# Optimization experiments

Measured on AMD Instinct MI355X. Metric: run time of the kernel, lower is better.

The kernel has to match this reference:

```python
import jax, jax.numpy as jnp
import numpy as np
from jax import lax

N = 5000
C = 81  # num_classes including background at index 0
BG_OFFSET = 1


def _iou_matrix(b):
    # b: [N,4] as x1,y1,x2,y2 -> pairwise IoU [N,N]
    x1, y1, x2, y2 = b[:, 0], b[:, 1], b[:, 2], b[:, 3]
    area = (x2 - x1) * (y2 - y1)  # [N]
    ix1 = jnp.maximum(x1[:, None], x1[None, :])
    iy1 = jnp.maximum(y1[:, None], y1[None, :])
    ix2 = jnp.minimum(x2[:, None], x2[None, :])
    iy2 = jnp.minimum(y2[:, None], y2[None, :])
    iw = jnp.maximum(ix2 - ix1, 0.0)
    ih = jnp.maximum(iy2 - iy1, 0.0)
    inter = iw * ih
    return inter / (area[:, None] + area[None, :] - inter)


def setup_inputs() -> dict:
    key = jax.random.key(0)
    k1, k2, k3 = jax.random.split(key, 3)
    # valid boxes: x1<x2, y1<y2 on a ~1024px canvas, size ~up to 256px
    xy1 = jax.random.uniform(k1, (N, 2), dtype=jnp.float32) * 1024.0
    wh = jax.random.uniform(k2, (N, 2), dtype=jnp.float32) * 256.0 + 1.0
    bboxes = jnp.concatenate([xy1, xy1 + wh], axis=1)  # [N,4]
    scores = jax.random.uniform(k3, (N, C), dtype=jnp.float32)  # [N,C]
    return {
        "bboxes": bboxes,
        "scores": scores,
        "conf_thresh": 0.6,
        "nms_thresh": 0.5,
        "max_instances": 300,
    }


def _multiclass_nms(bboxes, scores, conf_thresh, nms_thresh, max_instances):
    n = bboxes.shape[0]
    neg_inf = jnp.finfo(scores.dtype).min
    iou = _iou_matrix(bboxes)  # [N,N]

    def nms_one_class(score_c):  # score_c: [N]
        valid = score_c > conf_thresh
        masked = jnp.where(valid, score_c, neg_inf)
        order = jnp.argsort(masked)[::-1]  # descending score

        def step(suppressed, idx):
            keep = valid[idx] & ~suppressed[idx]
            new_sup = jnp.where(keep, suppressed | (iou[idx] > nms_thresh), suppressed)
            return new_sup, keep

        _, keeps = lax.scan(step, jnp.zeros((n,), bool), order)
        # scatter keep flags back to original box order
        return jnp.zeros((n,), bool).at[order].set(keeps)

    fg_scores = scores[:, BG_OFFSET:].T  # [C-1, N]
    keep = jax.vmap(nms_one_class)(fg_scores)  # [C-1, N]

    # global top-k over all (class, box) kept detections, sorted by score desc
    flat = jnp.where(keep, fg_scores, neg_inf).reshape(-1)  # [(C-1)*N]
    top_scores, top_idx = lax.top_k(flat, max_instances)
    cls = top_idx // n + BG_OFFSET  # [K]
    box = top_idx % n  # [K]
    valid_out = top_scores > neg_inf / 2

    sel_score = scores[box, cls]  # differentiable gather
    preds = jnp.concatenate([bboxes[box], sel_score[:, None]], axis=1)  # [K,5]
    preds = jnp.where(valid_out[:, None], preds, 0.0)
    labels = jnp.where(valid_out, cls, -1)
    return preds, labels


def reference(bboxes, scores, conf_thresh, nms_thresh, max_instances):
    return _multiclass_nms(bboxes, scores, conf_thresh, nms_thresh, max_instances)
```

## Files before the change

### kernel.cpp

```cpp
#include <hip/hip_runtime.h>

typedef unsigned long long u64;
typedef unsigned int u32;
typedef unsigned short u16;

#define MSORT 4096
#define TPB1  1024
#define TPBF  1024
#define BOXCAP 3648
#define KCAP  3072
#define RSLOT_W 10
#define KPC   300
#define SELCAP 1024
#define PREFR 64
#define TBOX  128

#define WG_SCOPE  __HIP_MEMORY_SCOPE_WORKGROUP
#define DEV_SCOPE __HIP_MEMORY_SCOPE_AGENT

__device__ __forceinline__ float boxArea(float4 b) {
    return __fmul_rn(__fsub_rn(b.z, b.x), __fsub_rn(b.w, b.y));
}

template<bool GE>
__device__ __forceinline__ bool iou_gt(float4 a, float area_a, float4 b, float area_b, double B) {
    float ix1 = fmaxf(a.x, b.x), iy1 = fmaxf(a.y, b.y);
    float ix2 = fminf(a.z, b.z), iy2 = fminf(a.w, b.w);
    float iw  = fmaxf(__fsub_rn(ix2, ix1), 0.0f);
    float ih  = fmaxf(__fsub_rn(iy2, iy1), 0.0f);
    float inter = __fmul_rn(iw, ih);
    float uni   = __fsub_rn(__fadd_rn(area_a, area_b), inter);
    return GE ? ((double)inter >= B * (double)uni) : ((double)inter > B * (double)uni);
}

__device__ __forceinline__ int scoreBin(u32 bits) {
    int b = (int)(bits >> 12) - 0x3F000;
    return b < 0 ? 0 : (b > 2047 ? 2047 : b);
}

__device__ __forceinline__ void bstar_wave0(
    const u32* __restrict__ hist, int target, int tid,
    int* __restrict__ outBs, int* __restrict__ outTot)
{
    if (tid < 64) {
        int s = 0;
        #pragma unroll
        for (int b = 0; b < 32; b++)
            s += (int)hist[(tid << 5) + ((b + tid) & 31)];
        #pragma unroll
        for (int d = 1; d < 64; d <<= 1) {
            int v = __shfl_down(s, d, 64);
            if (tid + d < 64) s += v;
        }
        u64 bal = __ballot(s >= target);
        int ch  = bal ? (63 - __builtin_clzll(bal)) : -1;
        int tot = __shfl(s, 0, 64);
        int bs  = 0;
        if (ch >= 0) {
            int accAbove = (ch < 63) ? __shfl(s, ch + 1, 64) : 0;
            int h = (tid < 32) ? (int)hist[(ch << 5) + tid] : 0;
            #pragma unroll
            for (int d = 1; d < 32; d <<= 1) {
                int v = __shfl_down(h, d, 64);
                if (tid + d < 32) h += v;
            }
            u64 bal2 = __ballot((tid < 32) && (accAbove + h >= target));
            bs = (ch << 5) + (63 - __builtin_clzll(bal2));
        }
        if (tid == 0) { *outBs = bs; if (outTot) *outTot = tot; }
    }
}

__global__ __launch_bounds__(1024) void transpose_kernel(
    const float* __restrict__ scores, int N, int C,
    float* __restrict__ scoresT, u32* __restrict__ gHist)
{
    __shared__ float tile[TBOX * 81];
    const int tid = threadIdx.x;
    const int b0  = blockIdx.x * TBOX;
    const int nb  = (N - b0 < TBOX) ? (N - b0) : TBOX;
    const int tot = nb * C;
    for (int e = tid; e < tot; e += 1024)
        tile[e] = scores[(size_t)b0 * C + e];
    __syncthreads();
    if (nb == TBOX) {
        const int wtot = C << 7;
        for (int o = tid; o < wtot; o += 1024) {
            int cls = o >> 7, j = o & (TBOX - 1);
            scoresT[(size_t)cls * N + b0 + j] = tile[j * C + cls];
        }
    } else {
        const int wtot = C * nb;
        for (int o = tid; o < wtot; o += 1024) {
            int cls = o / nb, j = o - cls * nb;
            scoresT[(size_t)cls * N + b0 + j] = tile[j * C + cls];
        }
    }
    if (blockIdx.x == 0)
        for (int h = tid; h < 2052; h += 1024) gHist[h] = 0;
}

template<bool GE>
__device__ __forceinline__ int prefix_nms_w0(
    const float* __restrict__ bboxes, const u64* __restrict__ sorted,
    int R, double B, int tid, int c, int N, u64* __restrict__ gkept_c,
    u32* __restrict__ gHist)
{
    u64 key = (tid < R) ? sorted[tid] : 0;
    float4 bx = make_float4(0.f, 0.f, 0.f, 0.f);
    if (tid < R) bx = ((const float4*)bboxes)[(u32)key];
    float ar = boxArea(bx);
    u64 supB = (R >= 64) ? 0ull : (~0ull << R);
    int nk = 0;
    int i = -1;
    for (;;) {
        u64 mask = (i >= 63) ? 0ull : (~0ull << (i + 1));
        u64 alive = ~supB & mask;
        if (!alive) break;
        i = (int)__builtin_ctzll(alive);
        float4 bi;
        bi.x = __shfl(bx.x, i, 64); bi.y = __shfl(bx.y, i, 64);
        bi.z = __shfl(bx.z, i, 64); bi.w = __shfl(bx.w, i, 64);
        float ai = boxArea(bi);
        if (tid == 0) {
            u64 ki = sorted[i];
            u32 flat = (u32)c * (u32)N + (u32)ki;
            gkept_c[nk] = (ki & 0xFFFFFFFF00000000ull) | (u32)(~flat);
        }
        nk++;
        bool sup = (tid > i) && iou_gt<GE>(bi, ai, bx, ar, B);
        supB |= __ballot(sup);
    }
    if (tid < R && !((supB >> tid) & 1ull))
        atomicAdd(&gHist[scoreBin((u32)(key >> 32))], 1u);
    return nk;
}

__global__ __launch_bounds__(TPB1, 1) void nms_select_kernel(
    const float* __restrict__ bboxes, const float* __restrict__ scoresT,
    const float* __restrict__ conf_ptr, const float* __restrict__ nms_ptr,
    int N, u64* __restrict__ gkept,
    u32* __restrict__ gK, u32* __restrict__ g65, u32* __restrict__ gPre,
    u32* __restrict__ gHist, u32* __restrict__ gNk)
{
    __shared__ u64 keys[KCAP];
    __shared__ u32 hist[2048];
    __shared__ u64 keybuf[256];
    __shared__ u64 sorted[66];
    __shared__ int cntS, ncollS, bstarS, nkS;

    const int tid  = threadIdx.x;
    const int lane = tid & 63;
    const int c    = blockIdx.x;
    const int cls  = c + 1;
    const float conf = *conf_ptr;
    const float nmsT = *nms_ptr;

    for (int b = tid; b < 2048; b += TPB1) hist[b] = 0;
    if (tid < 66) sorted[tid] = 0;
    if (tid == 0) { cntS = 0; ncollS = 0; nkS = 0; }
    __syncthreads();

    const float* rowT = scoresT + (size_t)cls * N;
    const float4* rowT4 = (const float4*)rowT;
    const int N4 = N >> 2;
    for (int i4 = tid; i4 < N4; i4 += TPB1) {
        float4 s4 = rowT4[i4];
        #pragma unroll
        for (int j = 0; j < 4; j++) {
            float s = (j == 0) ? s4.x : (j == 1) ? s4.y : (j == 2) ? s4.z : s4.w;
            bool pass = (s > conf);
            u64 m = __ballot(pass);
            if (m) {
                int leader = (int)__builtin_ctzll(m);
                int base = 0;
                if (lane == leader) base = atomicAdd(&cntS, __popcll(m));
                base = __shfl(base, leader, 64);
                if (pass) {
                    int p = base + (int)__popcll(m & ((1ull << lane) - 1ull));
                    if (p < KCAP)
                        keys[p] = ((u64)__float_as_uint(s) << 32) | (u32)((i4 << 2) + j);
                    atomicAdd(&hist[scoreBin(__float_as_uint(s))], 1u);
                }
            }
        }
    }
    for (int i = (N4 << 2) + tid; i < N; i += TPB1) {
        float s = rowT[i];
        if (s > conf) {
            int p = atomicAdd(&cntS, 1);
            if (p < KCAP) keys[p] = ((u64)__float_as_uint(s) << 32) | (u32)i;
            atomicAdd(&hist[scoreBin(__float_as_uint(s))], 1u);
        }
    }
    __syncthreads();
    const int K = cntS;
    const bool preOv = (K > KCAP);
    const int target = K < (PREFR + 1) ? K : (PREFR + 1);

    bstar_wave0(hist, target, tid, &bstarS, nullptr);
    __syncthreads();
    const u32 tbits = (bstarS == 0) ? 0u : (((u32)bstarS + 0x3F000u) << 12);

    const int KL = K < KCAP ? K : KCAP;
    for (int p = tid; p < KL; p += TPB1) {
        u64 k = keys[p];
        bool pass = ((u32)(k >> 32) >= tbits);
        u64 m = __ballot(pass);
        if (m) {
            int leader = (int)__builtin_ctzll(m);
            int base = 0;
            if (lane == leader) base = atomicAdd(&ncollS, (int)__popcll(m));
            base = __shfl(base, leader, 64);
            if (pass) {
                int pos = base + (int)__popcll(m & ((1ull << lane) - 1ull));
                if (pos < 256) keybuf[pos] = k;
            }
        }
    }
    __syncthreads();
    const int ncoll = ncollS;
    const bool pre = preOv || (ncoll > 256);
    for (int p = ncoll + tid; p < 256; p += TPB1) keybuf[p] = 0;
    __syncthreads();

    u64* gkept_c = gkept + (size_t)c * KPC;
    if (!pre) {
        if (tid < 256) {
            u64 my = keybuf[tid];
            int rank = 0;
            for (int j = 0; j < 256; j++) rank += (keybuf[j] > my);
            if (my && rank < PREFR + 1) sorted[rank] = my;
        }
        __syncthreads();
        const u32 tb = __float_as_uint(nmsT);
        const float Tn = __uint_as_float(tb + 1u);
        const double B = ((double)nmsT + (double)Tn) * 0.5;
        const bool geCmp = (((tb + 1u) & 1u) == 0u);
        if (tid < 64) {
            int R = ncoll < PREFR ? ncoll : PREFR;
            int nk = geCmp ? prefix_nms_w0<true >(bboxes, sorted, R, B, tid, c, N, gkept_c, gHist)
                           : prefix_nms_w0<false>(bboxes, sorted, R, B, tid, c, N, gkept_c, gHist);
            if (tid == 0) nkS = nk;
        }
        __syncthreads();
    }
    if (tid == 0) {
        gK[c]   = (u32)K;
        g65[c]  = pre ? 0xFFFFFFFFu : ((ncoll >= PREFR + 1) ? (u32)(sorted[PREFR] >> 32) : 0u);
        gPre[c] = pre ? 1u : 0u;
        gNk[c]  = pre ? 0u : (u32)nkS;
    }
}

template<bool GE>
__device__ __forceinline__ u64 sweep_own(
    float4 bi, float area_i, const float4 (&breg)[RSLOT_W],
    const float (&areaj)[RSLOT_W], const float4* __restrict__ boxesLds,
    int base, int nslots, int lane, double B)
{
    u64 ns = 0;
    #pragma unroll
    for (int t = 0; t < RSLOT_W; t++)
        ns |= ((u64)iou_gt<GE>(bi, area_i, breg[t], areaj[t], B)) << (base + t);
    for (int t = RSLOT_W; t < nslots; t++) {
        float4 bj = boxesLds[((base + t) << 6) | lane];
        ns |= ((u64)iou_gt<GE>(bi, area_i, bj, boxArea(bj), B)) << (base + t);
    }
    return ns;
}

template<bool GE>
__device__ __forceinline__ int greedy_full(
    const float4* __restrict__ boxesLds, u16* __restrict__ keptR,
    float4* __restrict__ pubBox, u32* __restrict__ ctl,
    const u32* __restrict__ gsi_c, const float* __restrict__ rowT,
    u32 thetaBits,
    int K, int smax, double B, int lane, int wave)
{
    const int SW   = (smax + 3) >> 2;
    const int base = (wave * SW < smax) ? wave * SW : smax;
    const int end  = (base + SW < smax) ? base + SW : smax;
    const int nslots = end - base;

    float4 breg[RSLOT_W];
    float  areaj[RSLOT_W];
    #pragma unroll
    for (int t = 0; t < RSLOT_W; t++) {
        float4 b = boxesLds[((base + t) << 6) | lane];
        breg[t] = b;
        areaj[t] = boxArea(b);
    }

    u64 sup;
    {
        int t = (lane < K) ? ((K - lane + 63) >> 6) : 0;
        sup = (t >= 64) ? 0ull : (~0ull << t);
    }

    u32 seen = 0;
    if (wave != 0) {
        for (;;) {
            u32 d  = __hip_atomic_load(&ctl[2], __ATOMIC_ACQUIRE, WG_SCOPE);
            u32 cn = __hip_atomic_load(&ctl[0], __ATOMIC_ACQUIRE, WG_SCOPE);
            bool prog = (seen < cn);
            while (seen < cn) {
                float4 bi = pubBox[seen]; seen++;
                sup |= sweep_own<GE>(bi, boxArea(bi), breg, areaj, boxesLds, base, nslots, lane, B);
            }
            if (d) return -1;
            u32 aw = __hip_atomic_load(&ctl[1], __ATOMIC_ACQUIRE, WG_SCOPE);
            if (aw == (u32)wave) {
                u32 cn2 = __hip_atomic_load(&ctl[0], __ATOMIC_ACQUIRE, WG_SCOPE);
                while (seen < cn2) {
                    float4 bi = pubBox[seen]; seen++;
                    sup |= sweep_own<GE>(bi, boxArea(bi), breg, areaj, boxesLds, base, nslots, lane, B);
                }
                break;
            }
            if (!prog) __builtin_amdgcn_s_sleep(1);
        }
    }

    u32 nk = seen;
    const u32 seen0 = seen;
    int scur = base - 1;
    float4 bcur = make_float4(0.f, 0.f, 0.f, 0.f);
    float  acur = 0.f;
    int js = base << 6;

    for (;;) {
        int s = js >> 6;
        while (s > scur) {
            scur++;
            if (scur < end) {
                bcur = boxesLds[(scur << 6) | lane];
                acur = boxArea(bcur);
                u64 bit = 0;
                for (u32 k = seen0; k < nk; k++) {
                    float4 bk = pubBox[k];
                    bit |= ((u64)iou_gt<GE>(bk, boxArea(bk), bcur, acur, B));
                }
                sup |= bit << scur;
            }
        }
        if (scur >= end) {
            if (wave == 3) {
                if (lane == 0) __hip_atomic_store(&ctl[2], 1u, __ATOMIC_RELEASE, WG_SCOPE);
                return (int)nk;
            }
            if (lane == 0) __hip_atomic_store(&ctl[1], (u32)(wave + 1), __ATOMIC_RELEASE, WG_SCOPE);
            return -1;
        }
        u64 bal = __ballot((int)(((~sup) >> scur) & 1ull)) & (~0ull << (js & 63));
        if (bal == 0) { js = (scur + 1) << 6; continue; }
        int i = (scur << 6) + (int)__builtin_ctzll(bal);

        if (thetaBits) {
            u32 idx = gsi_c[i];
            float sc = rowT[idx];
            if (__float_as_uint(sc) < thetaBits) {
                if (lane == 0) __hip_atomic_store(&ctl[2], 1u, __ATOMIC_RELEASE, WG_SCOPE);
                return (int)nk;
            }
        }
        float4 bi = boxesLds[i];
        if (lane == 0) { pubBox[nk] = bi; keptR[nk] = (u16)i; }
        nk++;
        if (nk >= KPC) {
            if (lane == 0) {
                __hip_atomic_store(&ctl[0], nk, __ATOMIC_RELEASE, WG_SCOPE);
                __hip_atomic_store(&ctl[2], 1u, __ATOMIC_RELEASE, WG_SCOPE);
            }
            return (int)nk;
        }
        if (lane == 0) __hip_atomic_store(&ctl[0], nk, __ATOMIC_RELEASE, WG_SCOPE);
        sup |= ((u64)iou_gt<GE>(bi, boxArea(bi), bcur, acur, B)) << scur;
        js = i + 1;
    }
}

__global__ __launch_bounds__(TPBF, 1) void nms_finale_kernel(
    const float* __restrict__ bboxes, const float* __restrict__ scoresT,
    const float* __restrict__ conf_ptr, const float* __restrict__ nms_ptr,
    int N, const u32* __restrict__ gHist,
    const u32* __restrict__ gK, const u32* __restrict__ g65, const u32* __restrict__ gPre,
    u32* __restrict__ gsi, u64* __restrict__ gkept,
    int Mout, float* __restrict__ out,
    u32* __restrict__ gDone, u32* __restrict__ gRerun, u32* __restrict__ gNk)
{
    __shared__ __align__(16) char smem[63856];
    __shared__ int cntS, lastS, selCountS, bs4S, thBs, thTot, nRerunS;

    const int c    = blockIdx.x;
    const int tid  = threadIdx.x;
    const int lane = tid & 63;

    u32* histT = (u32*)smem;
    for (int b = tid; b < 2048; b += TPBF) histT[b] = gHist[b];
    __syncthreads();
    bstar_wave0(histT, Mout, tid, &thBs, &thTot);
    __syncthreads();
    const int  thBsL = thBs;
    const u32 thetaBits = (thTot >= Mout && thBsL > 0) ? (((u32)thBsL + 0x3F000u) << 12) : 0u;
    u32 need = gPre[c];
    if (gK[c] > PREFR && g65[c] >= thetaBits) need = 1u;
    __syncthreads();

    u64* gkept_c = gkept + (size_t)c * KPC;

    if (need) {
        if (tid == 0) atomicAdd(gRerun, 1u);

        u64*    sortbuf  = (u64*)smem;
        float4* boxesLds = (float4*)smem;
        u16*    keptR    = (u16*)(smem + 58368);
        u32*    ctl      = (u32*)(smem + 58976);
        float4* pubBox   = (float4*)(smem + 58992);

        const int cls = c + 1;
        const float conf = *conf_ptr;
        const float nmsT = *nms_ptr;

        if (tid == 0) cntS = 0;
        __syncthreads();
        const float* rowT = scoresT + (size_t)cls * N;
        const float4* rowT4 = (const float4*)rowT;
        const int N4 = N >> 2;
        for (int i4 = tid; i4 < N4; i4 += TPBF) {
            float4 s4 = rowT4[i4];
            #pragma unroll
            for (int j = 0; j < 4; j++) {
                float s = (j == 0) ? s4.x : (j == 1) ? s4.y : (j == 2) ? s4.z : s4.w;
                bool pass = (s > conf);
                u64 m = __ballot(pass);
                if (m) {
                    int leader = (int)__builtin_ctzll(m);
                    int base = 0;
                    if (lane == leader) base = atomicAdd(&cntS, __popcll(m));
                    base = __shfl(base, leader, 64);
                    if (pass) {
                        int p = base + (int)__popcll(m & ((1ull << lane) - 1ull));
                        if (p < MSORT)
                            sortbuf[p] = ((u64)__float_as_uint(s) << 32) | (u32)((i4 << 2) + j);
                    }
                }
            }
        }
        for (int i = (N4 << 2) + tid; i < N; i += TPBF) {
            float s = rowT[i];
            if (s > conf) {
                int p = atomicAdd(&cntS, 1);
                if (p < MSORT) sortbuf[p] = ((u64)__float_as_uint(s) << 32) | (u32)i;
            }
        }
        __syncthreads();
        int K = cntS; if (K > BOXCAP) K = BOXCAP;
        int M = 64; while (M < K) M <<= 1;
        for (int p = K + tid; p < M; p += TPBF) sortbuf[p] = 0;
        __syncthreads();
        for (int kk = 2; kk <= M; kk <<= 1) {
            for (int j = kk >> 1; j > 0; j >>= 1) {
                for (int i = tid; i < M; i += TPBF) {
                    int ixj = i ^ j;
                    if (ixj > i) {
                        u64 a = sortbuf[i], b = sortbuf[ixj];
                        if (((i & kk) == 0) ? (a < b) : (a > b)) { sortbuf[i] = b; sortbuf[ixj] = a; }
                    }
                }
                __syncthreads();
            }
        }
        u32 myIdx[MSORT / TPBF];
        #pragma unroll
        for (int t = 0; t < MSORT / TPBF; t++) myIdx[t] = (u32)sortbuf[t * TPBF + tid];
        __syncthreads();
        u32* gsi_c = gsi + (size_t)c * BOXCAP;
        #pragma unroll
        for (int t = 0; t < MSORT / TPBF; t++) {
            int r = t * TPBF + tid;
            if (r < K) {
                u32 idx = myIdx[t];
                gsi_c[r] = idx;
                boxesLds[r] = ((const float4*)bboxes)[idx];
            }
        }
        if (tid == 0) { ctl[0] = 0; ctl[1] = 0; ctl[2] = 0; }
        __syncthreads();

        if (tid < 256) {
            const int wave = tid >> 6;
            const u32 tb = __float_as_uint(nmsT);
            const float Tn = __uint_as_float(tb + 1u);
            const double B = ((double)nmsT + (double)Tn) * 0.5;
            const bool geCmp = (((tb + 1u) & 1u) == 0u);
            const int smax = (K + 63) >> 6;

            int ret = geCmp ? greedy_full<true >(boxesLds, keptR, pubBox, ctl, gsi_c, rowT, thetaBits, K, smax, B, lane, wave)
                            : greedy_full<false>(boxesLds, keptR, pubBox, ctl, gsi_c, rowT, thetaBits, K, smax, B, lane, wave);
            if (ret >= 0) {
                int kept = ret; if (kept > KPC) kept = KPC;
                for (int p = lane; p < kept; p += 64) {
                    int rank = keptR[p];
                    u32 idx = gsi_c[rank];
                    float sc = rowT[idx];
                    u32 flat = (u32)c * (u32)N + idx;
                    gkept_c[p] = ((u64)__float_as_uint(sc) << 32) | (u32)(~flat);
                }
                if (lane == 0) gNk[c] = (u32)kept;
            }
        }
    }

    __syncthreads();
    if (tid == 0) {
        u32 v = need ? __hip_atomic_fetch_add(gDone, 1u, __ATOMIC_RELEASE, DEV_SCOPE)
                     : __hip_atomic_fetch_add(gDone, 1u, __ATOMIC_RELAXED, DEV_SCOPE);
        lastS = (v == (u32)(gridDim.x - 1)) ? 1 : 0;
    }
    __syncthreads();
    if (!lastS) return;
    if (tid == 0) {
        __hip_atomic_fetch_add(gDone, 0u, __ATOMIC_ACQUIRE, DEV_SCOPE);
        nRerunS = (int)__hip_atomic_load(gRerun, __ATOMIC_ACQUIRE, DEV_SCOPE);
    }
    __syncthreads();

    u64* selL  = (u64*)smem;
    u32* hist4 = (u32*)(smem + 8192);
    u32* nkL   = (u32*)(smem + 16384);
    const int nc = (int)gridDim.x;
    const int total = nc * KPC;

    for (int c2 = tid; c2 < nc; c2 += TPBF) nkL[c2] = gNk[c2];
    __syncthreads();

    int bstar;
    if (nRerunS == 0) {
        bstar = thBsL;
    } else {
        for (int b = tid; b < 2048; b += TPBF) hist4[b] = 0;
        __syncthreads();
        for (int t = tid; t < total; t += TPBF) {
            int cc = t / KPC, j = t - cc * KPC;
            if (j < (int)nkL[cc]) {
                u64 k = gkept[t];
                atomicAdd(&hist4[scoreBin((u32)(k >> 32))], 1u);
            }
        }
        __syncthreads();
        bstar_wave0(hist4, Mout, tid, &bs4S, nullptr);
        __syncthreads();
        bstar = bs4S;
    }

    if (tid == 0) selCountS = 0;
    __syncthreads();
    for (int t = tid; t < total; t += TPBF) {
        int cc = t / KPC, j = t - cc * KPC;
        bool pass = (j < (int)nkL[cc]);
        u64 k = 0;
        if (pass) {
            k = gkept[t];
            pass = (scoreBin((u32)(k >> 32)) >= bstar);
        }
        u64 m = __ballot(pass);
        if (m) {
            int leader = (int)__builtin_ctzll(m);
            int base = 0;
            if (lane == leader) base = atomicAdd(&selCountS, (int)__popcll(m));
            base = __shfl(base, leader, 64);
            if (pass) {
                int p = base + (int)__popcll(m & ((1ull << lane) - 1ull));
                if (p < SELCAP) selL[p] = k;
            }
        }
    }
    __syncthreads();
    int cnt = selCountS; if (cnt > SELCAP) cnt = SELCAP;

    if (cnt < Mout) {
        for (int t = tid; t < Mout; t += TPBF) {
            out[t * 5 + 0] = 0.f; out[t * 5 + 1] = 0.f; out[t * 5 + 2] = 0.f;
            out[t * 5 + 3] = 0.f; out[t * 5 + 4] = 0.f;
            out[Mout * 5 + t] = -1.0f;
        }
    }
    __syncthreads();
    if (tid < cnt) {
        u64 my = selL[tid];
        int rank = 0;
        for (int j = 0; j < cnt; j++) rank += (selL[j] > my);
        if (rank < Mout) {
            float s  = __uint_as_float((u32)(my >> 32));
            u32 flat = ~((u32)my);
            int cc   = (int)(flat / (u32)N);
            int box  = (int)(flat - (u32)cc * (u32)N);
            float4 bb = ((const float4*)bboxes)[box];
            out[rank * 5 + 0] = bb.x;
            out[rank * 5 + 1] = bb.y;
            out[rank * 5 + 2] = bb.z;
            out[rank * 5 + 3] = bb.w;
            out[rank * 5 + 4] = s;
            out[Mout * 5 + rank] = (float)(cc + 1);
        }
    }
}

extern "C" void kernel_launch(void* const* d_in, const int* in_sizes, int n_in,
                              void* d_out, int out_size, void* d_ws, size_t ws_size,
                              hipStream_t stream) {
    const float* bboxes = (const float*)d_in[0];
    const float* scores = (const float*)d_in[1];
    const float* conf   = (const float*)d_in[2];
    const float* nmsT   = (const float*)d_in[3];

    const int N    = in_sizes[0] / 4;
    const int C    = in_sizes[1] / N;
    const int nc   = C - 1;
    const int Mout = out_size / 6;

    char* wsb = (char*)d_ws;
    size_t off = 0;
    float* scoresT = (float*)(wsb + off); off += ((size_t)C * N * sizeof(float) + 255) & ~(size_t)255;
    u32* gsi   = (u32*)(wsb + off); off += (size_t)nc * BOXCAP * sizeof(u32);
    u64* gkept = (u64*)(wsb + off); off += (size_t)nc * KPC * sizeof(u64);
    u32* gK    = (u32*)(wsb + off); off += (size_t)((nc + 1) & ~1) * sizeof(u32);
    u32* g65   = (u32*)(wsb + off); off += (size_t)((nc + 1) & ~1) * sizeof(u32);
    u32* gPre  = (u32*)(wsb + off); off += (size_t)((nc + 1) & ~1) * sizeof(u32);
    u32* gHist = (u32*)(wsb + off); off += 2052 * sizeof(u32);
    u32* gDone  = gHist + 2048;
    u32* gRerun = gHist + 2049;
    u32* gNk   = (u32*)(wsb + off); off += (size_t)((nc + 1) & ~1) * sizeof(u32);

    const int ntile = (N + TBOX - 1) / TBOX;
    transpose_kernel<<<ntile, 1024, 0, stream>>>(scores, N, C, scoresT, gHist);
    nms_select_kernel<<<nc, TPB1, 0, stream>>>(bboxes, scoresT, conf, nmsT, N,
                                               gkept, gK, g65, gPre, gHist, gNk);
    nms_finale_kernel<<<nc, TPBF, 0, stream>>>(bboxes, scoresT, conf, nmsT, N,
                                               gHist, gK, g65, gPre, gsi, gkept,
                                               Mout, (float*)d_out, gDone, gRerun, gNk);
}
```

Baseline: 111.7 us.

## Fuse score transpose into per-class select kernel and recompute kept histogram in finale

Drops the separate transpose kernel: each class block now scans the full row-major score matrix, extracts its own column into LDS, writes the transposed row for later use, and filters from LDS. The global kept-score histogram built with atomics in the prefix NMS is removed; instead every finale block rebuilds it from the kept lists. Counter reset moves into the select kernel. This removes one launch and global atomics, but each block now reads the whole score matrix and duplicates the histogram work.

```diff
diff --git a/kernel.cpp b/kernel.cpp
--- a/kernel.cpp
+++ b/kernel.cpp
@@ -13,7 +13,7 @@
 #define KPC   300
 #define SELCAP 1024
 #define PREFR 64
-#define TBOX  128
+#define NMAX  5120
 
 #define WG_SCOPE  __HIP_MEMORY_SCOPE_WORKGROUP
 #define DEV_SCOPE __HIP_MEMORY_SCOPE_AGENT
@@ -71,40 +71,10 @@
     }
 }
 
-__global__ __launch_bounds__(1024) void transpose_kernel(
-    const float* __restrict__ scores, int N, int C,
-    float* __restrict__ scoresT, u32* __restrict__ gHist)
-{
-    __shared__ float tile[TBOX * 81];
-    const int tid = threadIdx.x;
-    const int b0  = blockIdx.x * TBOX;
-    const int nb  = (N - b0 < TBOX) ? (N - b0) : TBOX;
-    const int tot = nb * C;
-    for (int e = tid; e < tot; e += 1024)
-        tile[e] = scores[(size_t)b0 * C + e];
-    __syncthreads();
-    if (nb == TBOX) {
-        const int wtot = C << 7;
-        for (int o = tid; o < wtot; o += 1024) {
-            int cls = o >> 7, j = o & (TBOX - 1);
-            scoresT[(size_t)cls * N + b0 + j] = tile[j * C + cls];
-        }
-    } else {
-        const int wtot = C * nb;
-        for (int o = tid; o < wtot; o += 1024) {
-            int cls = o / nb, j = o - cls * nb;
-            scoresT[(size_t)cls * N + b0 + j] = tile[j * C + cls];
-        }
-    }
-    if (blockIdx.x == 0)
-        for (int h = tid; h < 2052; h += 1024) gHist[h] = 0;
-}
-
 template<bool GE>
 __device__ __forceinline__ int prefix_nms_w0(
     const float* __restrict__ bboxes, const u64* __restrict__ sorted,
-    int R, double B, int tid, int c, int N, u64* __restrict__ gkept_c,
-    u32* __restrict__ gHist)
+    int R, double B, int tid, int c, int N, u64* __restrict__ gkept_c)
 {
     u64 key = (tid < R) ? sorted[tid] : 0;
     float4 bx = make_float4(0.f, 0.f, 0.f, 0.f);
@@ -131,20 +101,19 @@
         bool sup = (tid > i) && iou_gt<GE>(bi, ai, bx, ar, B);
         supB |= __ballot(sup);
     }
-    if (tid < R && !((supB >> tid) & 1ull))
-        atomicAdd(&gHist[scoreBin((u32)(key >> 32))], 1u);
     return nk;
 }
 
 __global__ __launch_bounds__(TPB1, 1) void nms_select_kernel(
-    const float* __restrict__ bboxes, const float* __restrict__ scoresT,
+    const float* __restrict__ bboxes, const float* __restrict__ scores,
     const float* __restrict__ conf_ptr, const float* __restrict__ nms_ptr,
-    int N, u64* __restrict__ gkept,
+    int N, int C, float* __restrict__ scoresT, u64* __restrict__ gkept,
     u32* __restrict__ gK, u32* __restrict__ g65, u32* __restrict__ gPre,
-    u32* __restrict__ gHist, u32* __restrict__ gNk)
+    u32* __restrict__ gNk, u32* __restrict__ gDone, u32* __restrict__ gRerun)
 {
     __shared__ u64 keys[KCAP];
     __shared__ u32 hist[2048];
+    __shared__ __align__(16) float rowL[NMAX];
     __shared__ u64 keybuf[256];
     __shared__ u64 sorted[66];
     __shared__ int cntS, ncollS, bstarS, nkS;
@@ -156,41 +125,76 @@
     const float conf = *conf_ptr;
     const float nmsT = *nms_ptr;
 
+    if (c == 0 && tid == 0) { *gDone = 0; *gRerun = 0; }
+
     for (int b = tid; b < 2048; b += TPB1) hist[b] = 0;
     if (tid < 66) sorted[tid] = 0;
     if (tid == 0) { cntS = 0; ncollS = 0; nkS = 0; }
     __syncthreads();
 
-    const float* rowT = scoresT + (size_t)cls * N;
-    const float4* rowT4 = (const float4*)rowT;
-    const int N4 = N >> 2;
-    for (int i4 = tid; i4 < N4; i4 += TPB1) {
-        float4 s4 = rowT4[i4];
-        #pragma unroll
-        for (int j = 0; j < 4; j++) {
-            float s = (j == 0) ? s4.x : (j == 1) ? s4.y : (j == 2) ? s4.z : s4.w;
-            bool pass = (s > conf);
-            u64 m = __ballot(pass);
-            if (m) {
-                int leader = (int)__builtin_ctzll(m);
-                int base = 0;
-                if (lane == leader) base = atomicAdd(&cntS, __popcll(m));
-                base = __shfl(base, leader, 64);
-                if (pass) {
-                    int p = base + (int)__popcll(m & ((1ull << lane) - 1ull));
-                    if (p < KCAP)
-                        keys[p] = ((u64)__float_as_uint(s) << 32) | (u32)((i4 << 2) + j);
-                    atomicAdd(&hist[scoreBin(__float_as_uint(s))], 1u);
+    float* rowT = scoresT + (size_t)cls * N;
+    const bool ldsPath = (N <= NMAX) && (C >= 4);
+
+    if (ldsPath) {
+        const float4* s4p = (const float4*)scores;
+        const int NC  = N * C;
+        const int NC4 = NC >> 2;
+        for (int q = tid; q < NC4; q += TPB1) {
+            float4 v = s4p[q];
+            int flat = q << 2;
+            int r = flat % C;
+            int j = cls - r; if (j < 0) j += C;
+            if (j < 4) {
+                float s = (j == 0) ? v.x : (j == 1) ? v.y : (j == 2) ? v.z : v.w;
+                rowL[(flat + j) / C] = s;
+            }
+        }
+        for (int f = (NC4 << 2) + tid; f < NC; f += TPB1)
+            if (f % C == cls) rowL[f / C] = scores[f];
+        __syncthreads();
+
+        for (int i = tid; i < N; i += TPB1) rowT[i] = rowL[i];
+
+        const float4* rowL4 = (const float4*)rowL;
+        const int N4 = N >> 2;
+        for (int i4 = tid; i4 < N4; i4 += TPB1) {
+            float4 s4 = rowL4[i4];
+            #pragma unroll
+            for (int j = 0; j < 4; j++) {
+                float s = (j == 0) ? s4.x : (j == 1) ? s4.y : (j == 2) ? s4.z : s4.w;
+                bool pass = (s > conf);
+                u64 m = __ballot(pass);
+                if (m) {
+                    int leader = (int)__builtin_ctzll(m);
+                    int base = 0;
+                    if (lane == leader) base = atomicAdd(&cntS, __popcll(m));
+                    base = __shfl(base, leader, 64);
+                    if (pass) {
+                        int p = base + (int)__popcll(m & ((1ull << lane) - 1ull));
+                        if (p < KCAP)
+                            keys[p] = ((u64)__float_as_uint(s) << 32) | (u32)((i4 << 2) + j);
+                        atomicAdd(&hist[scoreBin(__float_as_uint(s))], 1u);
+                    }
                 }
             }
         }
-    }
-    for (int i = (N4 << 2) + tid; i < N; i += TPB1) {
-        float s = rowT[i];
-        if (s > conf) {
-            int p = atomicAdd(&cntS, 1);
-            if (p < KCAP) keys[p] = ((u64)__float_as_uint(s) << 32) | (u32)i;
-            atomicAdd(&hist[scoreBin(__float_as_uint(s))], 1u);
+        for (int i = (N4 << 2) + tid; i < N; i += TPB1) {
+            float s = rowL[i];
+            if (s > conf) {
+                int p = atomicAdd(&cntS, 1);
+                if (p < KCAP) keys[p] = ((u64)__float_as_uint(s) << 32) | (u32)i;
+                atomicAdd(&hist[scoreBin(__float_as_uint(s))], 1u);
+            }
+        }
+    } else {
+        for (int i = tid; i < N; i += TPB1) {
+            float s = scores[(size_t)i * C + cls];
+            rowT[i] = s;
+            if (s > conf) {
+                int p = atomicAdd(&cntS, 1);
+                if (p < KCAP) keys[p] = ((u64)__float_as_uint(s) << 32) | (u32)i;
+                atomicAdd(&hist[scoreBin(__float_as_uint(s))], 1u);
+            }
         }
     }
     __syncthreads();
@@ -239,8 +243,8 @@
         const bool geCmp = (((tb + 1u) & 1u) == 0u);
         if (tid < 64) {
             int R = ncoll < PREFR ? ncoll : PREFR;
-            int nk = geCmp ? prefix_nms_w0<true >(bboxes, sorted, R, B, tid, c, N, gkept_c, gHist)
-                           : prefix_nms_w0<false>(bboxes, sorted, R, B, tid, c, N, gkept_c, gHist);
+            int nk = geCmp ? prefix_nms_w0<true >(bboxes, sorted, R, B, tid, c, N, gkept_c)
+                           : prefix_nms_w0<false>(bboxes, sorted, R, B, tid, c, N, gkept_c);
             if (tid == 0) nkS = nk;
         }
         __syncthreads();
@@ -383,8 +387,8 @@
 __global__ __launch_bounds__(TPBF, 1) void nms_finale_kernel(
     const float* __restrict__ bboxes, const float* __restrict__ scoresT,
     const float* __restrict__ conf_ptr, const float* __restrict__ nms_ptr,
-    int N, const u32* __restrict__ gHist,
-    const u32* __restrict__ gK, const u32* __restrict__ g65, const u32* __restrict__ gPre,
+    int N, const u32* __restrict__ gK, const u32* __restrict__ g65,
+    const u32* __restrict__ gPre,
     u32* __restrict__ gsi, u64* __restrict__ gkept,
     int Mout, float* __restrict__ out,
     u32* __restrict__ gDone, u32* __restrict__ gRerun, u32* __restrict__ gNk)
@@ -395,12 +399,26 @@
     const int c    = blockIdx.x;
     const int tid  = threadIdx.x;
     const int lane = tid & 63;
-
-    u32* histT = (u32*)smem;
-    for (int b = tid; b < 2048; b += TPBF) histT[b] = gHist[b];
-    __syncthreads();
-    bstar_wave0(histT, Mout, tid, &thBs, &thTot);
-    __syncthreads();
+    const int nc   = (int)gridDim.x;
+    const int total = nc * KPC;
+
+    {
+        u32* histT = (u32*)smem;
+        u32* nkT   = (u32*)(smem + 8192);
+        for (int b = tid; b < 2048; b += TPBF) histT[b] = 0;
+        for (int c2 = tid; c2 < nc; c2 += TPBF) nkT[c2] = gNk[c2];
+        __syncthreads();
+        for (int t = tid; t < total; t += TPBF) {
+            int cc = t / KPC, j = t - cc * KPC;
+            if (j < (int)nkT[cc]) {
+                u64 k = gkept[t];
+                atomicAdd(&histT[scoreBin((u32)(k >> 32))], 1u);
+            }
+        }
+        __syncthreads();
+        bstar_wave0(histT, Mout, tid, &thBs, &thTot);
+        __syncthreads();
+    }
     const int  thBsL = thBs;
     const u32 thetaBits = (thTot >= Mout && thBsL > 0) ? (((u32)thBsL + 0x3F000u) << 12) : 0u;
     u32 need = gPre[c];
@@ -529,8 +547,6 @@
     u64* selL  = (u64*)smem;
     u32* hist4 = (u32*)(smem + 8192);
     u32* nkL   = (u32*)(smem + 16384);
-    const int nc = (int)gridDim.x;
-    const int total = nc * KPC;
 
     for (int c2 = tid; c2 < nc; c2 += TPBF) nkL[c2] = gNk[c2];
     __syncthreads();
@@ -628,16 +644,14 @@
     u32* gK    = (u32*)(wsb + off); off += (size_t)((nc + 1) & ~1) * sizeof(u32);
     u32* g65   = (u32*)(wsb + off); off += (size_t)((nc + 1) & ~1) * sizeof(u32);
     u32* gPre  = (u32*)(wsb + off); off += (size_t)((nc + 1) & ~1) * sizeof(u32);
-    u32* gHist = (u32*)(wsb + off); off += 2052 * sizeof(u32);
-    u32* gDone  = gHist + 2048;
-    u32* gRerun = gHist + 2049;
     u32* gNk   = (u32*)(wsb + off); off += (size_t)((nc + 1) & ~1) * sizeof(u32);
-
-    const int ntile = (N + TBOX - 1) / TBOX;
-    transpose_kernel<<<ntile, 1024, 0, stream>>>(scores, N, C, scoresT, gHist);
-    nms_select_kernel<<<nc, TPB1, 0, stream>>>(bboxes, scoresT, conf, nmsT, N,
-                                               gkept, gK, g65, gPre, gHist, gNk);
+    u32* gDone  = (u32*)(wsb + off); off += sizeof(u32);
+    u32* gRerun = (u32*)(wsb + off); off += sizeof(u32);
+
+    nms_select_kernel<<<nc, TPB1, 0, stream>>>(bboxes, scores, conf, nmsT, N, C,
+                                               scoresT, gkept, gK, g65, gPre,
+                                               gNk, gDone, gRerun);
     nms_finale_kernel<<<nc, TPBF, 0, stream>>>(bboxes, scoresT, conf, nmsT, N,
-                                               gHist, gK, g65, gPre, gsi, gkept,
+                                               gK, g65, gPre, gsi, gkept,
                                                Mout, (float*)d_out, gDone, gRerun, gNk);
 }
```

Result: slower. 150.5 us (+34.7%).
